# Optimization experiments

Hardware: AMD Instinct MI355X
Metric: run time of the kernel (lower is better)

Reference implementation:

```python
import jax, jax.numpy as jnp
import numpy as np

DIM = 1024
HEAD_DIM = 64
NUM_HEADS = DIM // HEAD_DIM
SCALE = HEAD_DIM ** -0.5


def setup_inputs() -> dict:
    key = jax.random.key(0)
    ks = jax.random.split(key, 12)
    b, n = 4, 2048
    std = DIM ** -0.5
    inp = {
        'words': jax.random.normal(ks[0], (b, n, DIM), jnp.float32),
        'position': jax.random.normal(ks[1], (b, n, DIM), jnp.float32),
        'conscious': jax.random.normal(ks[2], (b, n, DIM), jnp.float32),
        # projection weights stored as [in, out] (torch Linear W^T)
        'w_wq': jax.random.normal(ks[3], (DIM, DIM), jnp.float32) * std,
        'w_wk': jax.random.normal(ks[4], (DIM, DIM), jnp.float32) * std,
        'w_wv': jax.random.normal(ks[5], (DIM, DIM), jnp.float32) * std,
        'w_pq': jax.random.normal(ks[6], (DIM, DIM), jnp.float32) * std,
        'w_pk': jax.random.normal(ks[7], (DIM, DIM), jnp.float32) * std,
        'w_cq': jax.random.normal(ks[8], (DIM, DIM), jnp.float32) * std,
        'w_ck': jax.random.normal(ks[9], (DIM, DIM), jnp.float32) * std,
        'w_out': jax.random.normal(ks[10], (DIM, DIM), jnp.float32) * std,
        'b_out': jax.random.normal(ks[11], (DIM,), jnp.float32) * 0.01,
    }
    return inp


def _heads(x):
    b, n, _ = x.shape
    return x.reshape(b, n, NUM_HEADS, HEAD_DIM).transpose(0, 2, 1, 3)  # b h n d


def reference(words, position, conscious, w_wq, w_wk, w_wv, w_pq, w_pk, w_cq, w_ck, w_out, b_out):
    # fused multi-source q/k: sum of three projections per source
    q = _heads(words @ w_wq + position @ w_pq + conscious @ w_cq)
    k = _heads(words @ w_wk + position @ w_pk + conscious @ w_ck)
    v = _heads(words @ w_wv)
    sim = jnp.einsum('bhid,bhjd->bhij', q, k) * SCALE
    attn = jax.nn.softmax(sim, axis=-1)
    out = jnp.einsum('bhij,bhjd->bhid', attn, v)
    b, h, n, d = out.shape
    out = out.transpose(0, 2, 1, 3).reshape(b, n, h * d)
    return out @ w_out + b_out
```

## Files before the change

### kernel.cpp

```cpp
#include <hip/hip_runtime.h>
#include <hip/hip_bf16.h>

typedef __bf16 bf16_t;
typedef __attribute__((ext_vector_type(8))) __bf16 bf16x8;
typedef __attribute__((ext_vector_type(4))) float f32x4;
typedef __attribute__((ext_vector_type(16))) float f32x16;

__device__ __forceinline__ void gld_lds16(const void* g, void* l) {
  __builtin_amdgcn_global_load_lds((const __attribute__((address_space(1))) void*)g,
                                   (__attribute__((address_space(3))) void*)l, 16, 0, 0);
}

__global__ __launch_bounds__(256) void cast_concat(
    const float* __restrict__ w, const float* __restrict__ p,
    const float* __restrict__ c, bf16_t* __restrict__ X)
{
  unsigned idx = blockIdx.x * 256u + threadIdx.x;
  unsigned src = idx >> 21;
  unsigned rem = idx & ((1u << 21) - 1);
  unsigned row = rem >> 8;
  unsigned k4  = (rem & 255u) * 4u;
  const float* s = (src == 0) ? w : (src == 1) ? p : c;
  f32x4 v = *(const f32x4*)(s + (size_t)row * 1024 + k4);
  ushort4 u;
  u.x = __builtin_bit_cast(unsigned short, (bf16_t)v[0]);
  u.y = __builtin_bit_cast(unsigned short, (bf16_t)v[1]);
  u.z = __builtin_bit_cast(unsigned short, (bf16_t)v[2]);
  u.w = __builtin_bit_cast(unsigned short, (bf16_t)v[3]);
  *(ushort4*)(X + (size_t)row * 3072 + src * 1024 + k4) = u;
}

__global__ __launch_bounds__(256) void transpose_all(
    const float* __restrict__ w_wq, const float* __restrict__ w_pq,
    const float* __restrict__ w_cq, const float* __restrict__ w_wk,
    const float* __restrict__ w_pk, const float* __restrict__ w_ck,
    const float* __restrict__ w_wv, const float* __restrict__ w_out,
    bf16_t* __restrict__ Wqkt, bf16_t* __restrict__ Wvt, bf16_t* __restrict__ Wot)
{
  __shared__ float t[32][33];
  const int z = blockIdx.z;
  const float* src; bf16_t* dst; int dstride, koff, roff;
  switch (z) {
    case 0: src = w_wq;  dst = Wqkt; dstride = 3072; koff = 0;    roff = 0;    break;
    case 1: src = w_pq;  dst = Wqkt; dstride = 3072; koff = 1024; roff = 0;    break;
    case 2: src = w_cq;  dst = Wqkt; dstride = 3072; koff = 2048; roff = 0;    break;
    case 3: src = w_wk;  dst = Wqkt; dstride = 3072; koff = 0;    roff = 1024; break;
    case 4: src = w_pk;  dst = Wqkt; dstride = 3072; koff = 1024; roff = 1024; break;
    case 5: src = w_ck;  dst = Wqkt; dstride = 3072; koff = 2048; roff = 1024; break;
    case 6: src = w_wv;  dst = Wvt;  dstride = 1024; koff = 0;    roff = 0;    break;
    default: src = w_out; dst = Wot; dstride = 1024; koff = 0;    roff = 0;    break;
  }
  int bx = blockIdx.x, by = blockIdx.y;
  int x = bx * 32 + threadIdx.x;
  int y0 = by * 32;
  for (int i = threadIdx.y; i < 32; i += 8)
    t[i][threadIdx.x] = src[(size_t)(y0 + i) * 1024 + x];
  __syncthreads();
  int n0 = bx * 32;
  for (int i = threadIdx.y; i < 32; i += 8)
    dst[(size_t)(n0 + i + roff) * dstride + koff + y0 + threadIdx.x] =
        (bf16_t)t[threadIdx.x][i];
}

__global__ __launch_bounds__(512, 2) void gemm256_qk(
    const bf16_t* __restrict__ A, int lda,
    const bf16_t* __restrict__ Bt, int K,
    bf16_t* __restrict__ Qo, bf16_t* __restrict__ Ko, float scale, int nbx)
{
  __shared__ bf16_t As[2][256 * 64];
  __shared__ bf16_t Bs[2][256 * 64];

  const int tid = threadIdx.x;
  const int wave = tid >> 6, lane = tid & 63;
  const int wm = wave >> 2, wn = wave & 3;
  const int lrow = lane & 15, lch = lane >> 4;

  const int nwg = gridDim.x, cpx = nwg >> 3;
  const int id  = blockIdx.x;
  const int swz = (id & 7) * cpx + (id >> 3);
  const int mb = swz / nbx, nb = swz % nbx;
  const int m0 = mb * 256, n0 = nb * 256;

  const int srow = tid >> 3, spp = tid & 7;

  auto STAGE = [&](int buf, int k0) {
#pragma unroll
    for (int i = 0; i < 4; ++i) {
      int r = i * 64 + srow;
      int gsw = (spp ^ (r & 7)) * 8;
      gld_lds16(A + (size_t)(m0 + r) * lda + k0 + gsw, &As[buf][r * 64 + spp * 8]);
    }
#pragma unroll
    for (int i = 0; i < 4; ++i) {
      int r = i * 64 + srow;
      int gsw = (spp ^ (r & 7)) * 8;
      gld_lds16(Bt + (size_t)(n0 + r) * K + k0 + gsw, &Bs[buf][r * 64 + spp * 8]);
    }
  };

  const int NT = K >> 6;
  STAGE(0, 0);
  STAGE(1, 64);

  f32x4 acc[8][4] = {};

  for (int kt = 0; kt < NT; ++kt) {
    const int cur = kt & 1;
    if (kt < NT - 1) {
      asm volatile("s_waitcnt vmcnt(8)" ::: "memory");
    } else {
      asm volatile("s_waitcnt vmcnt(0)" ::: "memory");
    }
    asm volatile("s_barrier" ::: "memory");

#pragma unroll
    for (int ks = 0; ks < 2; ++ks) {
      bf16x8 af[8], bfr[4];
#pragma unroll
      for (int m = 0; m < 8; ++m) {
        int r = wm * 128 + m * 16 + lrow;
        af[m] = *(const bf16x8*)&As[cur][r * 64 + (((ks * 4 + lch) ^ (r & 7)) * 8)];
      }
#pragma unroll
      for (int n = 0; n < 4; ++n) {
        int r = wn * 64 + n * 16 + lrow;
        bfr[n] = *(const bf16x8*)&Bs[cur][r * 64 + (((ks * 4 + lch) ^ (r & 7)) * 8)];
      }
      __builtin_amdgcn_s_setprio(1);
#pragma unroll
      for (int m = 0; m < 8; ++m)
#pragma unroll
        for (int n = 0; n < 4; ++n)
          acc[m][n] = __builtin_amdgcn_mfma_f32_16x16x32_bf16(af[m], bfr[n], acc[m][n], 0, 0, 0);
      __builtin_amdgcn_s_setprio(0);
    }

    asm volatile("s_waitcnt lgkmcnt(0)" ::: "memory");
    asm volatile("s_barrier" ::: "memory");
    if (kt + 2 < NT) STAGE(cur, (kt + 2) * 64);
  }

  const int g = lane >> 4, cl = lane & 15;
#pragma unroll
  for (int m = 0; m < 8; ++m) {
    int m_base = m0 + wm * 128 + m * 16 + g * 4;
    int bb = m_base >> 11, nn = m_base & 2047;
#pragma unroll
    for (int n = 0; n < 4; ++n) {
      int col = n0 + wn * 64 + n * 16 + cl;
      bf16_t* dst = (col < 1024) ? Qo : Ko;
      int cc2 = col & 1023;
      float sc = (col < 1024) ? scale : 1.0f;
      int h = cc2 >> 6, d = cc2 & 63;
      size_t base = ((size_t)(bb * 16 + h) * 2048 + nn) * 64 + d;
#pragma unroll
      for (int r = 0; r < 4; ++r)
        dst[base + (size_t)r * 64] = (bf16_t)(acc[m][n][r] * sc);
    }
  }
}

template<int EPI>
__global__ __launch_bounds__(512, 2) void gemm128x256(
    const bf16_t* __restrict__ A, int lda,
    const bf16_t* __restrict__ Bt, int K,
    void* __restrict__ Cout, const float* __restrict__ bias)
{
  __shared__ bf16_t As[2][128 * 64];
  __shared__ bf16_t Bs[2][256 * 64];

  const int tid = threadIdx.x;
  const int wave = tid >> 6, lane = tid & 63;
  const int wm = wave >> 2, wn = wave & 3;
  const int lrow = lane & 15, lch = lane >> 4;

  const int nwg = gridDim.x, cpx = nwg >> 3;
  const int id  = blockIdx.x;
  const int swz = (id & 7) * cpx + (id >> 3);
  const int mb = swz >> 2, nb = swz & 3;
  const int m0 = mb * 128, n0 = nb * 256;

  const int srow = tid >> 3, spp = tid & 7;

  auto STAGE = [&](int buf, int k0) {
#pragma unroll
    for (int i = 0; i < 2; ++i) {
      int r = i * 64 + srow;
      int gsw = (spp ^ (r & 7)) * 8;
      gld_lds16(A + (size_t)(m0 + r) * lda + k0 + gsw, &As[buf][r * 64 + spp * 8]);
    }
#pragma unroll
    for (int i = 0; i < 4; ++i) {
      int r = i * 64 + srow;
      int gsw = (spp ^ (r & 7)) * 8;
      gld_lds16(Bt + (size_t)(n0 + r) * K + k0 + gsw, &Bs[buf][r * 64 + spp * 8]);
    }
  };

  const int NT = K >> 6;
  STAGE(0, 0);
  STAGE(1, 64);

  f32x4 acc[4][4] = {};

  for (int kt = 0; kt < NT; ++kt) {
    const int cur = kt & 1;
    if (kt < NT - 1) {
      asm volatile("s_waitcnt vmcnt(6)" ::: "memory");
    } else {
      asm volatile("s_waitcnt vmcnt(0)" ::: "memory");
    }
    asm volatile("s_barrier" ::: "memory");

#pragma unroll
    for (int ks = 0; ks < 2; ++ks) {
      bf16x8 af[4], bfr[4];
#pragma unroll
      for (int m = 0; m < 4; ++m) {
        int r = wm * 64 + m * 16 + lrow;
        af[m] = *(const bf16x8*)&As[cur][r * 64 + (((ks * 4 + lch) ^ (r & 7)) * 8)];
      }
#pragma unroll
      for (int n = 0; n < 4; ++n) {
        int r = wn * 64 + n * 16 + lrow;
        bfr[n] = *(const bf16x8*)&Bs[cur][r * 64 + (((ks * 4 + lch) ^ (r & 7)) * 8)];
      }
      __builtin_amdgcn_s_setprio(1);
#pragma unroll
      for (int m = 0; m < 4; ++m)
#pragma unroll
        for (int n = 0; n < 4; ++n)
          acc[m][n] = __builtin_amdgcn_mfma_f32_16x16x32_bf16(af[m], bfr[n], acc[m][n], 0, 0, 0);
      __builtin_amdgcn_s_setprio(0);
    }

    asm volatile("s_waitcnt lgkmcnt(0)" ::: "memory");
    asm volatile("s_barrier" ::: "memory");
    if (kt + 2 < NT) STAGE(cur, (kt + 2) * 64);
  }

  const int g = lane >> 4, cl = lane & 15;
  if (EPI == 1) {
    bf16_t* Vo = (bf16_t*)Cout;
#pragma unroll
    for (int m = 0; m < 4; ++m) {
      int m_base = m0 + wm * 64 + m * 16 + g * 4;
      int bb = m_base >> 11, nn = m_base & 2047;
#pragma unroll
      for (int n = 0; n < 4; ++n) {
        int col = n0 + wn * 64 + n * 16 + cl;
        int h = col >> 6, d = col & 63;
        ushort4 u;
        u.x = __builtin_bit_cast(unsigned short, (bf16_t)acc[m][n][0]);
        u.y = __builtin_bit_cast(unsigned short, (bf16_t)acc[m][n][1]);
        u.z = __builtin_bit_cast(unsigned short, (bf16_t)acc[m][n][2]);
        u.w = __builtin_bit_cast(unsigned short, (bf16_t)acc[m][n][3]);
        *(ushort4*)(Vo + ((size_t)(bb * 16 + h) * 64 + d) * 2048 + nn) = u;
      }
    }
  } else {
    float* Co = (float*)Cout;
#pragma unroll
    for (int m = 0; m < 4; ++m) {
      int m_base = m0 + wm * 64 + m * 16 + g * 4;
#pragma unroll
      for (int n = 0; n < 4; ++n) {
        int col = n0 + wn * 64 + n * 16 + cl;
        float bv = bias[col];
#pragma unroll
        for (int r = 0; r < 4; ++r)
          Co[(size_t)(m_base + r) * 1024 + col] = acc[m][n][r] + bv;
      }
    }
  }
}

__global__ __launch_bounds__(512, 2) void attn_kernel(
    const bf16_t* __restrict__ Q, const bf16_t* __restrict__ Kb,
    const bf16_t* __restrict__ Vt, bf16_t* __restrict__ O)
{
  __shared__ bf16_t Ks[2][64 * 64];
  __shared__ bf16_t Vs[2][64 * 64];

  const int fid = blockIdx.x;
  const int swz = (fid & 7) * 64 + (fid >> 3);
  const int bh = swz >> 3, qt = swz & 7;
  const int bb = bh >> 4, h = bh & 15;

  const int tid = threadIdx.x, wave = tid >> 6, lane = tid & 63;
  const int lq = lane & 31;
  const int lh = lane >> 5;

  const bf16_t* Qb    = Q  + ((size_t)bh * 2048 + qt * 256) * 64;
  const bf16_t* Kbase = Kb + (size_t)bh * 2048 * 64;
  const bf16_t* Vbase = Vt + (size_t)bh * 64 * 2048;

  auto STAGE = [&](int buf, int kv0) {
    int row = tid >> 3, pp = tid & 7;
    int sgr = (pp ^ (row & 7)) * 8;
    gld_lds16(Kbase + (size_t)(kv0 + row) * 64 + sgr, &Ks[buf][tid * 8]);
    gld_lds16(Vbase + (size_t)row * 2048 + kv0 + sgr, &Vs[buf][tid * 8]);
  };

  STAGE(0, 0);

  bf16x8 qf[4];
#pragma unroll
  for (int kf = 0; kf < 4; ++kf)
    qf[kf] = *(const bf16x8*)(Qb + (size_t)(wave * 32 + lq) * 64 + kf * 16 + lh * 8);

  f32x16 acc[2] = {};
  float m_run = -1.0e30f, l_run = 0.f;

  for (int t = 0; t < 32; ++t) {
    const int buf = t & 1;
    if (t < 31) {
      STAGE(buf ^ 1, (t + 1) * 64);
      asm volatile("s_waitcnt vmcnt(2)" ::: "memory");
    } else {
      asm volatile("s_waitcnt vmcnt(0)" ::: "memory");
    }
    __builtin_amdgcn_s_barrier();
    asm volatile("" ::: "memory");

    f32x16 st[2] = {};
#pragma unroll
    for (int nb = 0; nb < 2; ++nb) {
      int r = nb * 32 + lq;
#pragma unroll
      for (int kf = 0; kf < 4; ++kf) {
        bf16x8 ka = *(const bf16x8*)&Ks[buf][r * 64 + (((kf * 2 + lh) ^ (r & 7)) * 8)];
        st[nb] = __builtin_amdgcn_mfma_f32_32x32x16_bf16(ka, qf[kf], st[nb], 0, 0, 0);
      }
    }

    float tmax = st[0][0];
#pragma unroll
    for (int nb = 0; nb < 2; ++nb)
#pragma unroll
      for (int rg = 0; rg < 16; ++rg)
        tmax = fmaxf(tmax, st[nb][rg]);
    tmax = fmaxf(tmax, __shfl_xor(tmax, 32));

    if (!__all(tmax <= m_run + 8.0f)) {
      float mnew = fmaxf(m_run, tmax);
      float corr = __builtin_amdgcn_exp2f(m_run - mnew);
      m_run = mnew;
      l_run *= corr;
#pragma unroll
      for (int db = 0; db < 2; ++db)
#pragma unroll
        for (int rg = 0; rg < 16; ++rg)
          acc[db][rg] *= corr;
    }

    float sm = 0.f;
#pragma unroll
    for (int nb = 0; nb < 2; ++nb)
#pragma unroll
      for (int rg = 0; rg < 16; ++rg) {
        float p = __builtin_amdgcn_exp2f(st[nb][rg] - m_run);
        st[nb][rg] = p;
        sm += p;
      }
    sm += __shfl_xor(sm, 32);
    l_run += sm;

#pragma unroll
    for (int ks = 0; ks < 4; ++ks) {
      const int nb = ks >> 1;
      const int R = (ks & 1) * 8;
      unsigned x0, x1, y0, y1;
      asm("v_cvt_pk_bf16_f32 %0, %1, %2" : "=v"(x0) : "v"(st[nb][R + 0]), "v"(st[nb][R + 1]));
      asm("v_cvt_pk_bf16_f32 %0, %1, %2" : "=v"(x1) : "v"(st[nb][R + 2]), "v"(st[nb][R + 3]));
      asm("v_cvt_pk_bf16_f32 %0, %1, %2" : "=v"(y0) : "v"(st[nb][R + 4]), "v"(st[nb][R + 5]));
      asm("v_cvt_pk_bf16_f32 %0, %1, %2" : "=v"(y1) : "v"(st[nb][R + 6]), "v"(st[nb][R + 7]));
      asm volatile("v_permlane32_swap_b32 %0, %1" : "+v"(x0), "+v"(y0));
      asm volatile("v_permlane32_swap_b32 %0, %1" : "+v"(x1), "+v"(y1));
      int4 pw;
      pw.x = (int)x0; pw.y = (int)x1; pw.z = (int)y0; pw.w = (int)y1;
      bf16x8 pb = __builtin_bit_cast(bf16x8, pw);
#pragma unroll
      for (int db = 0; db < 2; ++db) {
        int r = db * 32 + lq;
        bf16x8 va = *(const bf16x8*)&Vs[buf][r * 64 + (((ks * 2 + lh) ^ (r & 7)) * 8)];
        acc[db] = __builtin_amdgcn_mfma_f32_32x32x16_bf16(va, pb, acc[db], 0, 0, 0);
      }
    }

    asm volatile("s_waitcnt lgkmcnt(0)" ::: "memory");
    __builtin_amdgcn_s_barrier();
    asm volatile("" ::: "memory");
  }

  float inv = 1.0f / l_run;
  int nn = qt * 256 + wave * 32 + lq;
  size_t obase = ((size_t)bb * 2048 + nn) * 1024 + h * 64;
#pragma unroll
  for (int db = 0; db < 2; ++db)
#pragma unroll
    for (int rr = 0; rr < 4; ++rr) {
      ushort4 u;
      u.x = __builtin_bit_cast(unsigned short, (bf16_t)(acc[db][rr * 4 + 0] * inv));
      u.y = __builtin_bit_cast(unsigned short, (bf16_t)(acc[db][rr * 4 + 1] * inv));
      u.z = __builtin_bit_cast(unsigned short, (bf16_t)(acc[db][rr * 4 + 2] * inv));
      u.w = __builtin_bit_cast(unsigned short, (bf16_t)(acc[db][rr * 4 + 3] * inv));
      *(ushort4*)(O + obase + db * 32 + rr * 8 + lh * 4) = u;
    }
}

extern "C" void kernel_launch(void* const* d_in, const int* in_sizes, int n_in,
                              void* d_out, int out_size, void* d_ws, size_t ws_size,
                              hipStream_t stream) {
  const float* words     = (const float*)d_in[0];
  const float* position  = (const float*)d_in[1];
  const float* conscious = (const float*)d_in[2];
  const float* w_wq  = (const float*)d_in[3];
  const float* w_wk  = (const float*)d_in[4];
  const float* w_wv  = (const float*)d_in[5];
  const float* w_pq  = (const float*)d_in[6];
  const float* w_pk  = (const float*)d_in[7];
  const float* w_cq  = (const float*)d_in[8];
  const float* w_ck  = (const float*)d_in[9];
  const float* w_out = (const float*)d_in[10];
  const float* b_out = (const float*)d_in[11];

  char* ws = (char*)d_ws;
  bf16_t* Xcat = (bf16_t*)(ws);
  bf16_t* Wqkt = (bf16_t*)(ws + 50331648);
  bf16_t* Wvt  = (bf16_t*)(ws + 62914560);
  bf16_t* Wot  = (bf16_t*)(ws + 65011712);
  bf16_t* Qb   = (bf16_t*)(ws + 67108864);
  bf16_t* Kbf  = (bf16_t*)(ws + 83886080);
  bf16_t* Vtb  = (bf16_t*)(ws + 100663296);
  bf16_t* Ob   = (bf16_t*)(ws + 117440512);

  cast_concat<<<24576, 256, 0, stream>>>(words, position, conscious, Xcat);

  transpose_all<<<dim3(32, 32, 8), dim3(32, 8), 0, stream>>>(
      w_wq, w_pq, w_cq, w_wk, w_pk, w_ck, w_wv, w_out, Wqkt, Wvt, Wot);

  gemm256_qk<<<256, 512, 0, stream>>>(Xcat, 3072, Wqkt, 3072, Qb, Kbf,
                                      0.125f * 1.44269504f, 8);
  gemm128x256<1><<<256, 512, 0, stream>>>(Xcat, 3072, Wvt, 1024, Vtb, nullptr);

  attn_kernel<<<512, 512, 0, stream>>>(Qb, Kbf, Vtb, Ob);

  gemm128x256<2><<<256, 512, 0, stream>>>(Ob, 1024, Wot, 1024, (float*)d_out, b_out);
}
```

Before: 288.9 us.

## Interleave A/B tile staging with MFMA phases in QK projection GEMM

Splits each k-tile iteration into four phases, each loading part of the A fragments and issuing half-tile async global-to-LDS loads between MFMA groups. A is now prefetched one tile ahead and B two tiles ahead, replacing the single bulk stage at the end of each iteration. The aim is to spread memory traffic across the compute and hide load latency. In exchange it adds extra barriers per iteration and relies on finer vmcnt accounting that is easy to get wrong.

```diff
diff --git a/kernel.cpp b/kernel.cpp
--- a/kernel.cpp
+++ b/kernel.cpp
@@ -83,61 +83,83 @@
 
   const int srow = tid >> 3, spp = tid & 7;
 
-  auto STAGE = [&](int buf, int k0) {
-#pragma unroll
-    for (int i = 0; i < 4; ++i) {
-      int r = i * 64 + srow;
+  auto STAGE_A = [&](int buf, int k0, int h) {
+#pragma unroll
+    for (int i = 0; i < 2; ++i) {
+      int r = h * 128 + i * 64 + srow;
       int gsw = (spp ^ (r & 7)) * 8;
       gld_lds16(A + (size_t)(m0 + r) * lda + k0 + gsw, &As[buf][r * 64 + spp * 8]);
     }
-#pragma unroll
-    for (int i = 0; i < 4; ++i) {
-      int r = i * 64 + srow;
+  };
+  auto STAGE_B = [&](int buf, int k0, int h) {
+#pragma unroll
+    for (int i = 0; i < 2; ++i) {
+      int r = h * 128 + i * 64 + srow;
       int gsw = (spp ^ (r & 7)) * 8;
       gld_lds16(Bt + (size_t)(n0 + r) * K + k0 + gsw, &Bs[buf][r * 64 + spp * 8]);
     }
   };
 
   const int NT = K >> 6;
-  STAGE(0, 0);
-  STAGE(1, 64);
+  STAGE_A(0, 0, 0); STAGE_A(0, 0, 1);
+  STAGE_B(0, 0, 0); STAGE_B(0, 0, 1);
+  STAGE_B(1, 64, 0); STAGE_B(1, 64, 1);
 
   f32x4 acc[8][4] = {};
 
   for (int kt = 0; kt < NT; ++kt) {
-    const int cur = kt & 1;
-    if (kt < NT - 1) {
-      asm volatile("s_waitcnt vmcnt(8)" ::: "memory");
-    } else {
-      asm volatile("s_waitcnt vmcnt(0)" ::: "memory");
-    }
-    asm volatile("s_barrier" ::: "memory");
-
-#pragma unroll
-    for (int ks = 0; ks < 2; ++ks) {
-      bf16x8 af[8], bfr[4];
-#pragma unroll
-      for (int m = 0; m < 8; ++m) {
-        int r = wm * 128 + m * 16 + lrow;
-        af[m] = *(const bf16x8*)&As[cur][r * 64 + (((ks * 4 + lch) ^ (r & 7)) * 8)];
-      }
-#pragma unroll
-      for (int n = 0; n < 4; ++n) {
-        int r = wn * 64 + n * 16 + lrow;
-        bfr[n] = *(const bf16x8*)&Bs[cur][r * 64 + (((ks * 4 + lch) ^ (r & 7)) * 8)];
+    const int cur = kt & 1, nxt = cur ^ 1;
+    bf16x8 bfr[4][2];
+
+#pragma unroll
+    for (int p = 0; p < 4; ++p) {
+      bf16x8 af[2][2];
+      if (p > 0) {
+#pragma unroll
+        for (int j = 0; j < 2; ++j)
+#pragma unroll
+          for (int ks = 0; ks < 2; ++ks) {
+            int r = wm * 128 + (p * 2 + j) * 16 + lrow;
+            af[j][ks] = *(const bf16x8*)&As[cur][r * 64 + (((ks * 4 + lch) ^ (r & 7)) * 8)];
+          }
+      }
+      if (p == 0 && kt + 1 < NT) STAGE_A(nxt, (kt + 1) * 64, 0);
+      if (p == 1 && kt + 1 < NT) STAGE_A(nxt, (kt + 1) * 64, 1);
+      if (p == 2 && kt + 2 < NT) STAGE_B(cur, (kt + 2) * 64, 0);
+      if (p == 3 && kt + 2 < NT) STAGE_B(cur, (kt + 2) * 64, 1);
+      if (p == 0) {
+        if (kt + 1 < NT) asm volatile("s_waitcnt vmcnt(6)" ::: "memory");
+        else             asm volatile("s_waitcnt vmcnt(0)" ::: "memory");
+      }
+      asm volatile("s_barrier" ::: "memory");
+      if (p == 0) {
+#pragma unroll
+        for (int j = 0; j < 2; ++j)
+#pragma unroll
+          for (int ks = 0; ks < 2; ++ks) {
+            int r = wm * 128 + j * 16 + lrow;
+            af[j][ks] = *(const bf16x8*)&As[cur][r * 64 + (((ks * 4 + lch) ^ (r & 7)) * 8)];
+          }
+#pragma unroll
+        for (int n = 0; n < 4; ++n)
+#pragma unroll
+          for (int ks = 0; ks < 2; ++ks) {
+            int r = wn * 64 + n * 16 + lrow;
+            bfr[n][ks] = *(const bf16x8*)&Bs[cur][r * 64 + (((ks * 4 + lch) ^ (r & 7)) * 8)];
+          }
       }
       __builtin_amdgcn_s_setprio(1);
 #pragma unroll
-      for (int m = 0; m < 8; ++m)
-#pragma unroll
-        for (int n = 0; n < 4; ++n)
-          acc[m][n] = __builtin_amdgcn_mfma_f32_16x16x32_bf16(af[m], bfr[n], acc[m][n], 0, 0, 0);
+      for (int ks = 0; ks < 2; ++ks)
+#pragma unroll
+        for (int j = 0; j < 2; ++j)
+#pragma unroll
+          for (int n = 0; n < 4; ++n)
+            acc[p * 2 + j][n] = __builtin_amdgcn_mfma_f32_16x16x32_bf16(
+                af[j][ks], bfr[n][ks], acc[p * 2 + j][n], 0, 0, 0);
       __builtin_amdgcn_s_setprio(0);
-    }
-
-    asm volatile("s_waitcnt lgkmcnt(0)" ::: "memory");
-    asm volatile("s_barrier" ::: "memory");
-    if (kt + 2 < NT) STAGE(cur, (kt + 2) * 64);
+      asm volatile("s_barrier" ::: "memory");
+    }
   }
 
   const int g = lane >> 4, cl = lane & 15;
```

Measured after the change: 292.8 us. About the same (+1.4%).

## Software-pipeline attention loop: overlap next tile QK^T with current PV

Applied to the files above, without the earlier changes.

Restructures the flash-attention inner loop so the QK^T MFMAs for tile t+1 are issued together with the PV MFMAs for tile t, and the softmax for t+1 runs afterwards. The goal is to keep the matrix units busy while the exp/max VALU work runs. K and V staging are split and offset by one tile, and s_setprio raises wave priority during the MFMA block. The cost is more live registers (scores held across iterations plus the pb fragments) and a more complex wait/barrier schedule.

```diff
diff --git a/kernel.cpp b/kernel.cpp
--- a/kernel.cpp
+++ b/kernel.cpp
@@ -295,14 +295,17 @@
   const bf16_t* Kbase = Kb + (size_t)bh * 2048 * 64;
   const bf16_t* Vbase = Vt + (size_t)bh * 64 * 2048;
 
-  auto STAGE = [&](int buf, int kv0) {
-    int row = tid >> 3, pp = tid & 7;
-    int sgr = (pp ^ (row & 7)) * 8;
-    gld_lds16(Kbase + (size_t)(kv0 + row) * 64 + sgr, &Ks[buf][tid * 8]);
-    gld_lds16(Vbase + (size_t)row * 2048 + kv0 + sgr, &Vs[buf][tid * 8]);
-  };
-
-  STAGE(0, 0);
+  const int srow = tid >> 3, spp = tid & 7;
+  const int sgr = (spp ^ (srow & 7)) * 8;
+
+  auto STAGE_K = [&](int buf, int tile) {
+    gld_lds16(Kbase + (size_t)(tile * 64 + srow) * 64 + sgr, &Ks[buf][tid * 8]);
+  };
+  auto STAGE_V = [&](int buf, int tile) {
+    gld_lds16(Vbase + (size_t)srow * 2048 + tile * 64 + sgr, &Vs[buf][tid * 8]);
+  };
+
+  STAGE_K(0, 0); STAGE_V(0, 0); STAGE_K(1, 1);
 
   bf16x8 qf[4];
 #pragma unroll
@@ -311,35 +314,42 @@
 
   f32x16 acc[2] = {};
   float m_run = -1.0e30f, l_run = 0.f;
-
-  for (int t = 0; t < 32; ++t) {
-    const int buf = t & 1;
-    if (t < 31) {
-      STAGE(buf ^ 1, (t + 1) * 64);
-      asm volatile("s_waitcnt vmcnt(2)" ::: "memory");
-    } else {
-      asm volatile("s_waitcnt vmcnt(0)" ::: "memory");
-    }
-    __builtin_amdgcn_s_barrier();
-    asm volatile("" ::: "memory");
-
-    f32x16 st[2] = {};
-#pragma unroll
-    for (int nb = 0; nb < 2; ++nb) {
-      int r = nb * 32 + lq;
+  bf16x8 pb[4];
+
+  auto QKT = [&](int tile, f32x16 (&st)[2]) {
+    const int kb = tile & 1;
+#pragma unroll
+    for (int nb2 = 0; nb2 < 2; ++nb2) {
+      int r = nb2 * 32 + lq;
+      f32x16 z = {};
 #pragma unroll
       for (int kf = 0; kf < 4; ++kf) {
-        bf16x8 ka = *(const bf16x8*)&Ks[buf][r * 64 + (((kf * 2 + lh) ^ (r & 7)) * 8)];
-        st[nb] = __builtin_amdgcn_mfma_f32_32x32x16_bf16(ka, qf[kf], st[nb], 0, 0, 0);
-      }
-    }
-
-    float tmax = st[0][0];
-#pragma unroll
-    for (int nb = 0; nb < 2; ++nb)
-#pragma unroll
-      for (int rg = 0; rg < 16; ++rg)
-        tmax = fmaxf(tmax, st[nb][rg]);
+        bf16x8 ka = *(const bf16x8*)&Ks[kb][r * 64 + (((kf * 2 + lh) ^ (r & 7)) * 8)];
+        z = __builtin_amdgcn_mfma_f32_32x32x16_bf16(ka, qf[kf], z, 0, 0, 0);
+      }
+      st[nb2] = z;
+    }
+  };
+
+  auto PV = [&](int tile) {
+    const int vb = tile & 1;
+#pragma unroll
+    for (int ks = 0; ks < 4; ++ks)
+#pragma unroll
+      for (int db = 0; db < 2; ++db) {
+        int r = db * 32 + lq;
+        bf16x8 va = *(const bf16x8*)&Vs[vb][r * 64 + (((ks * 2 + lh) ^ (r & 7)) * 8)];
+        acc[db] = __builtin_amdgcn_mfma_f32_32x32x16_bf16(va, pb[ks], acc[db], 0, 0, 0);
+      }
+  };
+
+  auto SOFTMAX = [&](f32x16 (&st)[2]) {
+    float tmax = fmaxf(st[0][0], st[0][1]);
+#pragma unroll
+    for (int nb2 = 0; nb2 < 2; ++nb2)
+#pragma unroll
+      for (int rg = (nb2 ? 0 : 2); rg < 16; rg += 2)
+        tmax = fmaxf(fmaxf(tmax, st[nb2][rg]), st[nb2][rg + 1]);
     tmax = fmaxf(tmax, __shfl_xor(tmax, 32));
 
     if (!__all(tmax <= m_run + 8.0f)) {
@@ -356,11 +366,11 @@
 
     float sm = 0.f;
 #pragma unroll
-    for (int nb = 0; nb < 2; ++nb)
+    for (int nb2 = 0; nb2 < 2; ++nb2)
 #pragma unroll
       for (int rg = 0; rg < 16; ++rg) {
-        float p = __builtin_amdgcn_exp2f(st[nb][rg] - m_run);
-        st[nb][rg] = p;
+        float p = __builtin_amdgcn_exp2f(st[nb2][rg] - m_run);
+        st[nb2][rg] = p;
         sm += p;
       }
     sm += __shfl_xor(sm, 32);
@@ -368,25 +378,48 @@
 
 #pragma unroll
     for (int ks = 0; ks < 4; ++ks) {
-      const int nb = ks >> 1;
+      const int nb2 = ks >> 1;
       const int R = (ks & 1) * 8;
       unsigned x0, x1, y0, y1;
-      asm("v_cvt_pk_bf16_f32 %0, %1, %2" : "=v"(x0) : "v"(st[nb][R + 0]), "v"(st[nb][R + 1]));
-      asm("v_cvt_pk_bf16_f32 %0, %1, %2" : "=v"(x1) : "v"(st[nb][R + 2]), "v"(st[nb][R + 3]));
-      asm("v_cvt_pk_bf16_f32 %0, %1, %2" : "=v"(y0) : "v"(st[nb][R + 4]), "v"(st[nb][R + 5]));
-      asm("v_cvt_pk_bf16_f32 %0, %1, %2" : "=v"(y1) : "v"(st[nb][R + 6]), "v"(st[nb][R + 7]));
+      asm("v_cvt_pk_bf16_f32 %0, %1, %2" : "=v"(x0) : "v"(st[nb2][R + 0]), "v"(st[nb2][R + 1]));
+      asm("v_cvt_pk_bf16_f32 %0, %1, %2" : "=v"(x1) : "v"(st[nb2][R + 2]), "v"(st[nb2][R + 3]));
+      asm("v_cvt_pk_bf16_f32 %0, %1, %2" : "=v"(y0) : "v"(st[nb2][R + 4]), "v"(st[nb2][R + 5]));
+      asm("v_cvt_pk_bf16_f32 %0, %1, %2" : "=v"(y1) : "v"(st[nb2][R + 6]), "v"(st[nb2][R + 7]));
       asm volatile("v_permlane32_swap_b32 %0, %1" : "+v"(x0), "+v"(y0));
       asm volatile("v_permlane32_swap_b32 %0, %1" : "+v"(x1), "+v"(y1));
       int4 pw;
       pw.x = (int)x0; pw.y = (int)x1; pw.z = (int)y0; pw.w = (int)y1;
-      bf16x8 pb = __builtin_bit_cast(bf16x8, pw);
-#pragma unroll
-      for (int db = 0; db < 2; ++db) {
-        int r = db * 32 + lq;
-        bf16x8 va = *(const bf16x8*)&Vs[buf][r * 64 + (((ks * 2 + lh) ^ (r & 7)) * 8)];
-        acc[db] = __builtin_amdgcn_mfma_f32_32x32x16_bf16(va, pb, acc[db], 0, 0, 0);
-      }
-    }
+      pb[ks] = __builtin_bit_cast(bf16x8, pw);
+    }
+  };
+
+  asm volatile("s_waitcnt vmcnt(0)" ::: "memory");
+  __builtin_amdgcn_s_barrier();
+  asm volatile("" ::: "memory");
+  {
+    f32x16 st[2];
+    QKT(0, st);
+    SOFTMAX(st);
+  }
+  asm volatile("s_waitcnt lgkmcnt(0)" ::: "memory");
+  __builtin_amdgcn_s_barrier();
+  asm volatile("" ::: "memory");
+
+  for (int t = 0; t < 32; ++t) {
+    if (t < 30)       { STAGE_V((t + 1) & 1, t + 1); STAGE_K(t & 1, t + 2); }
+    else if (t == 30) { STAGE_V(1, 31); }
+    if (t < 30)       asm volatile("s_waitcnt vmcnt(2)" ::: "memory");
+    else if (t == 30) asm volatile("s_waitcnt vmcnt(1)" ::: "memory");
+    else              asm volatile("s_waitcnt vmcnt(0)" ::: "memory");
+    __builtin_amdgcn_s_barrier();
+    asm volatile("" ::: "memory");
+
+    f32x16 st[2];
+    __builtin_amdgcn_s_setprio(1);
+    if (t < 31) QKT(t + 1, st);
+    PV(t);
+    __builtin_amdgcn_s_setprio(0);
+    if (t < 31) SOFTMAX(st);
 
     asm volatile("s_waitcnt lgkmcnt(0)" ::: "memory");
     __builtin_amdgcn_s_barrier();
```

Result: no change. 288.6 us (-0.1%).
